# Optimization experiments

Measured on AMD Instinct MI355X. Metric: run time of the kernel, lower is better.

Reference implementation:

```python
import jax, jax.numpy as jnp
import numpy as np

N, E, IN, H, T = 100000, 1600000, 10, 64, 10


def setup_inputs() -> dict:
    key = jax.random.key(0)
    ks = jax.random.split(key, 24)
    w = lambda k, shape, s=0.05: jax.random.normal(k, shape, jnp.float32) * s
    return {
        "x": w(ks[0], (N, IN), 1.0),
        "edge_attr": w(ks[1], (E, T), 1.0),
        "gcn1_w": w(ks[2], (IN, H)), "gcn1_b": jnp.zeros((H,), jnp.float32),
        "e_w1": w(ks[3], (3 * T, H)), "e_b1": jnp.zeros((H,), jnp.float32),
        "e_w2": w(ks[4], (H, H)), "e_b2": jnp.zeros((H,), jnp.float32),
        "gcn2_w": w(ks[5], (2 * H, H)), "gcn2_b": jnp.zeros((H,), jnp.float32),
        "gcn3_w": w(ks[6], (H, IN)), "gcn3_b": jnp.zeros((IN,), jnp.float32),
        "l1_w": w(ks[7], (2 * IN, IN)), "l1_b": jnp.zeros((IN,), jnp.float32),
        "l2_w": w(ks[8], (IN, 128)), "l2_b": jnp.zeros((128,), jnp.float32),
        "l3_w": w(ks[9], (128, 32)), "l3_b": jnp.zeros((32,), jnp.float32),
        "l4_w": w(ks[10], (32, 2)), "l4_b": jnp.zeros((2,), jnp.float32),
        "edge_index": jax.random.randint(ks[11], (2, E), 0, N),
    }


def reference(x, edge_attr, gcn1_w, gcn1_b, e_w1, e_b1, e_w2, e_b2,
              gcn2_w, gcn2_b, gcn3_w, gcn3_b, l1_w, l1_b, l2_w, l2_b,
              l3_w, l3_b, l4_w, l4_b, edge_index):
    src, dst = edge_index[0], edge_index[1]  # j -> i (message flows src->dst)
    # GCN symmetric norm with self loops: deg counted on target, +1 self loop
    deg = 1.0 + jax.ops.segment_sum(jnp.ones((E,), jnp.float32), dst, num_segments=N)
    dis = deg ** -0.5  # [N]
    edge_norm = (dis[src] * dis[dst])[:, None]  # [E,1]

    def gcn(h, w, b):
        hw = h @ w  # [N,out]
        agg = jax.ops.segment_sum(hw[src] * edge_norm, dst, num_segments=N)
        agg = agg + hw * (dis * dis)[:, None]  # self-loop term, norm = 1/deg
        return agg + b

    out1 = jax.nn.relu(gcn(x, gcn1_w, gcn1_b))
    # EdgeConv: gather x_i (dst), x_j (src), concat edge_attr, MLP, scatter-max
    m = jnp.concatenate([x[dst], x[src], edge_attr], axis=1)  # [E, 3T]
    m = jax.nn.relu(m @ e_w1 + e_b1) @ e_w2 + e_b2  # [E, H]
    agg = jax.ops.segment_max(m, dst, num_segments=N)
    agg = jnp.where(jnp.isfinite(agg), agg, 0.0)  # isolated nodes -> 0
    oute = jax.nn.relu(agg)

    out2 = jax.nn.relu(gcn(jnp.concatenate([out1, oute], axis=1), gcn2_w, gcn2_b))
    out3 = jax.nn.relu(gcn(out2, gcn3_w, gcn3_b))
    h = jnp.concatenate([x, out3], axis=1)  # [N, 2*IN]
    h = jax.nn.softplus(h @ l1_w + l1_b)
    h = jax.nn.softplus(h @ l2_w + l2_b)
    h = jax.nn.softplus(h @ l3_w + l3_b)
    h = h @ l4_w + l4_b  # [N, 2]
    return (h[:, 0], h[:, 1])
```

## Files before the change

### kernel.cpp

```cpp
#include <hip/hip_runtime.h>
#include <hip/hip_bf16.h>

typedef unsigned int u32;
typedef unsigned short u16;
typedef _Float16 f16;
typedef _Float16 f16x8 __attribute__((ext_vector_type(8)));
typedef float f32x4 __attribute__((ext_vector_type(4)));
typedef u32 u32x4 __attribute__((ext_vector_type(4)));

#define DEV static __device__ __forceinline__

#define O_G1   0
#define O_G1b  640
#define O_W1   704
#define O_B1   2624
#define O_W2   2688
#define O_B2   6784
#define O_G2   6848
#define O_G2b  15040
#define O_G3   15104
#define O_G3b  15744
#define O_L1   15754
#define O_L1b  15954
#define O_L2t  15964
#define O_L2b  17244
#define O_L3   17372
#define O_L3b  21468
#define O_L4t  21500
#define O_L4b  21564
#define O_WF1  21568
#define O_WF2  22592
#define WTOT   24640

#define ECNB   32

DEV float bfu(u16 h){ return __uint_as_float(((u32)h) << 16); }
DEV float bflo(u32 u){ return __uint_as_float(u << 16); }
DEV float bfhi(u32 u){ return __uint_as_float(u & 0xffff0000u); }
DEV u16 f2bf(float x){
  __hip_bfloat16 b = __float2bfloat16(x);
  return *(u16*)&b;
}
DEV float rdf(const void* p, int idx, int isf32){
  return isf32 ? ((const float*)p)[idx] : bfu(((const u16*)p)[idx]);
}
DEV void load10_bf(const u32* __restrict__ p, float* f){
  u32 a0=p[0],a1=p[1],a2=p[2],a3=p[3],a4=p[4];
  f[0]=bflo(a0); f[1]=bfhi(a0);
  f[2]=bflo(a1); f[3]=bfhi(a1);
  f[4]=bflo(a2); f[5]=bfhi(a2);
  f[6]=bflo(a3); f[7]=bfhi(a3);
  f[8]=bflo(a4); f[9]=bfhi(a4);
}
DEV void load10_any(const void* base, size_t row, int isf32, float* f){
  if (isf32){
    const float* p = (const float*)base + row*10;
    #pragma unroll
    for (int k=0;k<10;k++) f[k] = p[k];
  } else {
    load10_bf((const u32*)base + row*5, f);
  }
}
DEV float softplusf(float x){ return fmaxf(x,0.f) + __logf(1.f + __expf(-fabsf(x))); }

DEV int permk(int k){
  if (k < 8)  return k;
  if (k < 16) return 10 + (k-8);
  if (k < 24) return 20 + (k-16);
  if (k == 24) return 8;
  if (k == 25) return 9;
  if (k == 26) return 18;
  if (k == 27) return 19;
  if (k == 28) return 28;
  if (k == 29) return 29;
  return -1;
}
DEV u32 packh2(float a, float b){
  union { f16 h[2]; u32 u; } t;
  t.h[0] = (f16)a; t.h[1] = (f16)b;
  return t.u;
}

__global__ __launch_bounds__(256) void k_detect(
    const u32* p0, const u32* p1, const u32* p2, const u32* p3,
    const u32* p4, const u32* p5, const u32* p6, const u32* p7,
    const u32* p8, const u32* p9, const u32* p10,const u32* p11,
    const u32* p12,const u32* p13,const u32* p14,const u32* p15,
    const u32* p16,const u32* p17,const u32* p18,const u32* p19,
    int* __restrict__ flags, int N_, int E_)
{
  int a = blockIdx.x;
  const u32* p;
  int elems;
  switch (a){
    case 0:  p=p0;  elems=N_*10; break;
    case 1:  p=p1;  elems=E_*10; break;
    case 2:  p=p2;  elems=640;  break;
    case 3:  p=p3;  elems=64;   break;
    case 4:  p=p4;  elems=1920; break;
    case 5:  p=p5;  elems=64;   break;
    case 6:  p=p6;  elems=4096; break;
    case 7:  p=p7;  elems=64;   break;
    case 8:  p=p8;  elems=8192; break;
    case 9:  p=p9;  elems=64;   break;
    case 10: p=p10; elems=640;  break;
    case 11: p=p11; elems=10;   break;
    case 12: p=p12; elems=200;  break;
    case 13: p=p13; elems=10;   break;
    case 14: p=p14; elems=1280; break;
    case 15: p=p15; elems=128;  break;
    case 16: p=p16; elems=4096; break;
    case 17: p=p17; elems=32;   break;
    case 18: p=p18; elems=64;   break;
    default: p=p19; elems=2;    break;
  }
  int nw = elems/2; if (nw > 512) nw = 512; if (nw < 1) nw = 1;
  int localA = 0, localZ = 0;
  for (int i=threadIdx.x; i<nw; i+=256){
    u32 w = p[i];
    u32 ex = (w >> 7) & 0xffu;
    if (ex >= 0x90u) localA++;
    if ((w & 0xffffu) == 0u) localZ++;
  }
  int packed = (localA << 16) | localZ;
  __shared__ int red[4];
  #pragma unroll
  for (int off=32; off; off>>=1) packed += __shfl_down(packed, off);
  if ((threadIdx.x & 63) == 0) red[threadIdx.x>>6] = packed;
  __syncthreads();
  if (threadIdx.x == 0){
    int s = red[0]+red[1]+red[2]+red[3];
    int sA = s >> 16, sZ = s & 0xffff;
    flags[a] = (sA * 16 >= nw || sZ * 4 >= nw * 3) ? 1 : 0;
  }
}

__global__ __launch_bounds__(256) void k_prep(
    const void* g1w, const void* g1b, const void* ew1, const void* eb1,
    const void* ew2, const void* eb2, const void* g2w, const void* g2b,
    const void* g3w, const void* g3b, const void* l1w, const void* l1b,
    const void* l2w, const void* l2b, const void* l3w, const void* l3b,
    const void* l4w, const void* l4b,
    const int* __restrict__ flags, float* __restrict__ W)
{
  int t = threadIdx.x;
  int f2=flags[2],f3=flags[3],f4=flags[4],f5=flags[5],f6=flags[6],f7=flags[7];
  int f8=flags[8],f9=flags[9],f10=flags[10],f11=flags[11],f12=flags[12],f13=flags[13];
  int f14=flags[14],f15=flags[15],f16=flags[16],f17=flags[17],f18=flags[18],f19=flags[19];
  for (int i=t;i<640;i+=256)  W[O_G1+i]  = rdf(g1w,i,f2);
  for (int i=t;i<64;i+=256)   W[O_G1b+i] = rdf(g1b,i,f3);
  for (int i=t;i<1920;i+=256) W[O_W1+i]  = rdf(ew1,i,f4);
  for (int i=t;i<64;i+=256)   W[O_B1+i]  = rdf(eb1,i,f5);
  for (int i=t;i<4096;i+=256) W[O_W2+i]  = rdf(ew2,i,f6);
  for (int i=t;i<64;i+=256)   W[O_B2+i]  = rdf(eb2,i,f7);
  for (int i=t;i<8192;i+=256) W[O_G2+i]  = rdf(g2w,i,f8);
  for (int i=t;i<64;i+=256)   W[O_G2b+i] = rdf(g2b,i,f9);
  for (int i=t;i<640;i+=256)  W[O_G3+i]  = rdf(g3w,i,f10);
  for (int i=t;i<10;i+=256)   W[O_G3b+i] = rdf(g3b,i,f11);
  for (int i=t;i<200;i+=256)  W[O_L1+i]  = rdf(l1w,i,f12);
  for (int i=t;i<10;i+=256)   W[O_L1b+i] = rdf(l1b,i,f13);
  for (int i=t;i<1280;i+=256){ int o=i/10,k=i-o*10; W[O_L2t+i]=rdf(l2w,k*128+o,f14); }
  for (int i=t;i<128;i+=256)  W[O_L2b+i] = rdf(l2b,i,f15);
  for (int i=t;i<4096;i+=256) W[O_L3+i]  = rdf(l3w,i,f16);
  for (int i=t;i<32;i+=256)   W[O_L3b+i] = rdf(l3b,i,f17);
  for (int i=t;i<64;i+=256){ int c=i>>5,j=i&31; W[O_L4t+i]=rdf(l4w,j*2+c,f18); }
  for (int i=t;i<2;i+=256)    W[O_L4b+i] = rdf(l4b,i,f19);
  u32* Wu = (u32*)W;
  for (int i=t;i<1024;i+=256){
    int l=i&63, q=(i>>6)&3, c=i>>8;
    int k0=(l>>4)*8+2*q, col=c*16+(l&15);
    int r0=permk(k0), r1=permk(k0+1);
    float v0 = (r0<0)?0.f:rdf(ew1,r0*64+col,f4);
    float v1 = (r1<0)?0.f:rdf(ew1,r1*64+col,f4);
    Wu[O_WF1+i] = packh2(v0,v1);
  }
  for (int i=t;i<2048;i+=256){
    int l=i&63, q=(i>>6)&3, h2=(i>>8)&1, c=i>>9;
    int k0=32*h2+(l>>4)*8+2*q, col=c*16+(l&15);
    Wu[O_WF2+i] = packh2(rdf(ew2,k0*64+col,f6), rdf(ew2,(k0+1)*64+col,f6));
  }
}

__global__ __launch_bounds__(256) void k_init(int* __restrict__ cnt, int N_)
{
  int i = blockIdx.x*256 + threadIdx.x;
  if (i < N_) cnt[i] = 0;
}

__global__ __launch_bounds__(256) void k_count(
    const int* __restrict__ ei, int* __restrict__ cnt,
    int* __restrict__ rank, int E_)
{
  int e = blockIdx.x*256 + threadIdx.x;
  if (e >= E_) return;
  rank[e] = atomicAdd(&cnt[ei[E_+e]], 1);
}

__global__ __launch_bounds__(1024) void k_bsum(const int* __restrict__ cnt, int* __restrict__ bsum, int N_)
{
  int i = blockIdx.x*1024 + threadIdx.x;
  int v = (i < N_) ? cnt[i] : 0;
  #pragma unroll
  for (int off=32; off; off>>=1) v += __shfl_down(v, off);
  __shared__ int ws_[16];
  if ((threadIdx.x & 63) == 0) ws_[threadIdx.x>>6] = v;
  __syncthreads();
  if (threadIdx.x == 0){
    int s = 0;
    #pragma unroll
    for (int j=0;j<16;j++) s += ws_[j];
    bsum[blockIdx.x] = s;
  }
}

__global__ __launch_bounds__(128) void k_scan_small(const int* __restrict__ bsum, int* __restrict__ boff, int NB)
{
  int t = threadIdx.x;
  int v = (t < NB) ? bsum[t] : 0;
  int lane = t & 63, w = t >> 6;
  int x = v;
  #pragma unroll
  for (int off=1; off<64; off<<=1){ int y=__shfl_up(x,off); if (lane>=off) x+=y; }
  __shared__ int t2[2];
  if (lane==63) t2[w]=x;
  __syncthreads();
  if (w==1) x += t2[0];
  boff[t] = x - v;
}

__global__ __launch_bounds__(1024) void k_scan_final(
    int* __restrict__ cnt, const int* __restrict__ boff,
    int* __restrict__ rp, float* __restrict__ dis, int N_, int E_)
{
  int i = blockIdx.x*1024 + threadIdx.x;
  int v = (i < N_) ? cnt[i] : 0;
  int lane = threadIdx.x & 63, w = threadIdx.x >> 6;
  int x = v;
  #pragma unroll
  for (int off=1; off<64; off<<=1){ int y=__shfl_up(x,off); if (lane>=off) x+=y; }
  __shared__ int wp[16];
  if (lane==63) wp[w]=x;
  __syncthreads();
  if (threadIdx.x==0){
    int run=0;
    #pragma unroll
    for (int j=0;j<16;j++){ int t=wp[j]; wp[j]=run; run+=t; }
  }
  __syncthreads();
  int incl = x + wp[w] + boff[blockIdx.x];
  if (i < N_){
    rp[i]  = incl - v;
    dis[i] = rsqrtf(1.f + (float)v);
  }
  if (i == 0) rp[N_] = E_;
}

__global__ __launch_bounds__(256) void k_fillpos(
    const int* __restrict__ ei, const int* __restrict__ rank,
    const int* __restrict__ rp, int* __restrict__ inv, int E_)
{
  int e = blockIdx.x*256 + threadIdx.x;
  if (e >= E_) return;
  int d = ei[E_+e];
  inv[rp[d] + rank[e]] = e;
}

__global__ __launch_bounds__(256) void k_fillcsr(
    const int* __restrict__ ei, const int* __restrict__ inv,
    int4* __restrict__ csr, int E_)
{
  int p = blockIdx.x*256 + threadIdx.x;
  if (p >= E_) return;
  int e = inv[p];
  csr[p] = make_int4(ei[e], e, ei[E_+e], 0);
}

#define EC_EMIT \
  if (run >= 0){ int bb = run*64 + x; \
    atomicMax(&nodemax[bb],    __float_as_int(e0)); \
    atomicMax(&nodemax[bb+16], __float_as_int(e1)); \
    atomicMax(&nodemax[bb+32], __float_as_int(e2)); \
    atomicMax(&nodemax[bb+48], __float_as_int(e3)); }
#define EC_STEP(DD, RR) { \
  float t0=fmaxf(mcv[0][RR],0.f), t1=fmaxf(mcv[1][RR],0.f), \
        t2=fmaxf(mcv[2][RR],0.f), t3=fmaxf(mcv[3][RR],0.f); \
  if (DD == run){ e0=fmaxf(e0,t0); e1=fmaxf(e1,t1); e2=fmaxf(e2,t2); e3=fmaxf(e3,t3); } \
  else { EC_EMIT; run = DD; e0=t0; e1=t1; e2=t2; e3=t3; } }

__global__ __launch_bounds__(256) void k_edgeconv(
    const void* __restrict__ xv, const void* __restrict__ eav,
    const int* __restrict__ rp, const int4* __restrict__ csr,
    const float* __restrict__ W, const int* __restrict__ flags,
    float* __restrict__ oute, int N_, int E_)
{
  __shared__ int nodemax[ECNB*64];
  __shared__ u32 hbuf[4][16*36];
  int tid = threadIdx.x;
  int l = tid & 63, wv = tid >> 6;
  int x = l & 15, g = l >> 4;
  int n0 = blockIdx.x * ECNB;
  if (n0 >= N_) return;
  int nend = n0 + ECNB; if (nend > N_) nend = N_;
  #pragma unroll
  for (int i=0;i<ECNB/4;i++) nodemax[i*256 + tid] = 0;
  int fx = flags[0], fea = flags[1];
  const u32* Wu = (const u32*)W;
  union FU { u32 u[4]; f16x8 v; };
  union HU { f16 h[8]; u32 u[4]; f16x8 v; };
  FU w1u[4];
  #pragma unroll
  for (int c=0;c<4;c++){
    #pragma unroll
    for (int q=0;q<4;q++) w1u[c].u[q] = Wu[O_WF1 + (c*4+q)*64 + l];
  }
  FU w2u[4][2];
  #pragma unroll
  for (int c=0;c<4;c++){
    #pragma unroll
    for (int h=0;h<2;h++){
      #pragma unroll
      for (int q=0;q<4;q++) w2u[c][h].u[q] = Wu[O_WF2 + ((c*2+h)*4+q)*64 + l];
    }
  }
  float b1v[4], b2v[4];
  #pragma unroll
  for (int c=0;c<4;c++){ b1v[c] = (W+O_B1)[c*16 + x]; b2v[c] = (W+O_B2)[c*16 + x]; }
  int pbase = rp[n0], pend = rp[nend];
  int ntiles = (pend - pbase + 15) >> 4;
  u32* hb = hbuf[wv];
  __syncthreads();

  for (int t = wv; t < ntiles; t += 4){
    int p0 = pbase + t*16;
    int eA = p0 + x; if (eA > E_-1) eA = E_-1;
    int4 ce = csr[eA];
    HU af;
    u32 exv = 0;
    if (g < 3){
      long row; const void* base; int isf;
      if (g==0){ row = ce.z; base = xv;  isf = fx; }
      else if (g==1){ row = ce.x; base = xv;  isf = fx; }
      else { row = ce.y; base = eav; isf = fea; }
      if (isf){
        const float* p = (const float*)base + row*10;
        #pragma unroll
        for (int j=0;j<8;j++) af.h[j] = (f16)p[j];
        exv = packh2(p[8], p[9]);
      } else {
        const u32* p = (const u32*)base + row*5;
        u32 a0=p[0],a1=p[1],a2=p[2],a3=p[3],a4=p[4];
        af.h[0]=(f16)bflo(a0); af.h[1]=(f16)bfhi(a0);
        af.h[2]=(f16)bflo(a1); af.h[3]=(f16)bfhi(a1);
        af.h[4]=(f16)bflo(a2); af.h[5]=(f16)bfhi(a2);
        af.h[6]=(f16)bflo(a3); af.h[7]=(f16)bfhi(a3);
        exv = packh2(bflo(a4), bfhi(a4));
      }
    }
    u32 ge0 = (u32)__shfl((int)exv, x);
    u32 ge1 = (u32)__shfl((int)exv, x+16);
    u32 ge2 = (u32)__shfl((int)exv, x+32);
    if (g == 3){ af.u[0]=ge0; af.u[1]=ge1; af.u[2]=ge2; af.u[3]=0; }
    int pe = p0 + 4*g;
    int dz = ce.z;
    int d0 = __shfl(dz, 4*g+0); d0 = (pe   < pend) ? d0 - n0 : -1;
    int d1 = __shfl(dz, 4*g+1); d1 = (pe+1 < pend) ? d1 - n0 : -1;
    int d2 = __shfl(dz, 4*g+2); d2 = (pe+2 < pend) ? d2 - n0 : -1;
    int d3 = __shfl(dz, 4*g+3); d3 = (pe+3 < pend) ? d3 - n0 : -1;
    f32x4 z = {0.f,0.f,0.f,0.f};
    f32x4 hc[4];
    #pragma unroll
    for (int c=0;c<4;c++)
      hc[c] = __builtin_amdgcn_mfma_f32_16x16x32_f16(af.v, w1u[c].v, z, 0, 0, 0);
    #pragma unroll
    for (int r=0;r<4;r++){
      u32 pk0,pk1,pk2,pk3;
      {
        float hv = fmaxf(hc[0][r] + b1v[0], 0.f);
        union { f16 h; u16 u; } cv; cv.h=(f16)hv; u32 mine=cv.u;
        u32 other=(u32)__shfl_xor((int)mine,1,64);
        pk0 = (x&1) ? (other|(mine<<16)) : (mine|(other<<16));
      }{
        float hv = fmaxf(hc[1][r] + b1v[1], 0.f);
        union { f16 h; u16 u; } cv; cv.h=(f16)hv; u32 mine=cv.u;
        u32 other=(u32)__shfl_xor((int)mine,1,64);
        pk1 = (x&1) ? (other|(mine<<16)) : (mine|(other<<16));
      }{
        float hv = fmaxf(hc[2][r] + b1v[2], 0.f);
        union { f16 h; u16 u; } cv; cv.h=(f16)hv; u32 mine=cv.u;
        u32 other=(u32)__shfl_xor((int)mine,1,64);
        pk2 = (x&1) ? (other|(mine<<16)) : (mine|(other<<16));
      }{
        float hv = fmaxf(hc[3][r] + b1v[3], 0.f);
        union { f16 h; u16 u; } cv; cv.h=(f16)hv; u32 mine=cv.u;
        u32 other=(u32)__shfl_xor((int)mine,1,64);
        pk3 = (x&1) ? (other|(mine<<16)) : (mine|(other<<16));
      }
      int edge = 4*g + r;
      int par = (x&1) ? 16 : 0;
      hb[edge*36 + par + (x>>1)]     = (x&1) ? pk2 : pk0;
      hb[edge*36 + 8 + par + (x>>1)] = (x&1) ? pk3 : pk1;
    }
    asm volatile("s_waitcnt lgkmcnt(0)" ::: "memory");
    HU a2f[2];
    #pragma unroll
    for (int h=0;h<2;h++){
      const u32x4* p = (const u32x4*)&hb[x*36 + g*4 + 16*h];
      u32x4 tv = *p;
      a2f[h].u[0]=tv[0]; a2f[h].u[1]=tv[1]; a2f[h].u[2]=tv[2]; a2f[h].u[3]=tv[3];
    }
    f32x4 mcv[4];
    #pragma unroll
    for (int c=0;c<4;c++){
      f32x4 bi = {b2v[c],b2v[c],b2v[c],b2v[c]};
      f32x4 acc = __builtin_amdgcn_mfma_f32_16x16x32_f16(a2f[0].v, w2u[c][0].v, bi, 0, 0, 0);
      mcv[c]    = __builtin_amdgcn_mfma_f32_16x16x32_f16(a2f[1].v, w2u[c][1].v, acc, 0, 0, 0);
    }
    int run = -2; float e0=0.f,e1=0.f,e2=0.f,e3=0.f;
    EC_STEP(d0,0) EC_STEP(d1,1) EC_STEP(d2,2) EC_STEP(d3,3)
    EC_EMIT;
  }
  __syncthreads();
  int tot = (nend - n0) * 64;
  for (int i = tid; i < tot; i += 256)
    oute[(size_t)n0*64 + i] = __int_as_float(nodemax[i]);
}

__global__ __launch_bounds__(256) void k_aggx(
    const void* __restrict__ xv, const int* __restrict__ rp,
    const int4* __restrict__ csr, const float* __restrict__ dis,
    const int* __restrict__ flags, float* __restrict__ sx, int N_)
{
  int i = blockIdx.x*256 + threadIdx.x;
  if (i >= N_) return;
  int fx = flags[0];
  float di = dis[i], d2 = di*di;
  float acc[10], ac2[10], tA[10], tB[10], tC[10], tD[10];
  load10_any(xv, (size_t)i, fx, tA);
  #pragma unroll
  for (int f=0;f<10;f++){ acc[f] = tA[f]*d2; ac2[f] = 0.f; }
  int b = rp[i], en = rp[i+1];
  int p = b;
  for (; p+3 < en; p += 4){
    int s0 = csr[p].x, s1 = csr[p+1].x, s2 = csr[p+2].x, s3 = csr[p+3].x;
    float m0 = dis[s0]*di, m1 = dis[s1]*di, m2 = dis[s2]*di, m3 = dis[s3]*di;
    load10_any(xv, (size_t)s0, fx, tA);
    load10_any(xv, (size_t)s1, fx, tB);
    load10_any(xv, (size_t)s2, fx, tC);
    load10_any(xv, (size_t)s3, fx, tD);
    #pragma unroll
    for (int f=0;f<10;f++){
      acc[f] = fmaf(tA[f], m0, acc[f]);
      ac2[f] = fmaf(tB[f], m1, ac2[f]);
      acc[f] = fmaf(tC[f], m2, acc[f]);
      ac2[f] = fmaf(tD[f], m3, ac2[f]);
    }
  }
  for (; p < en; p++){
    int s0 = csr[p].x; float m0 = dis[s0]*di;
    load10_any(xv, (size_t)s0, fx, tA);
    #pragma unroll
    for (int f=0;f<10;f++) acc[f] = fmaf(tA[f], m0, acc[f]);
  }
  float* o = sx + (size_t)i*10;
  #pragma unroll
  for (int f=0;f<10;f++) o[f] = acc[f] + ac2[f];
}

__global__ __launch_bounds__(256) void k_hw2(
    const float* __restrict__ sx, const float* __restrict__ oute,
    const float* __restrict__ W, u16* __restrict__ hw2o, int N_)
{
  int i = blockIdx.x*256 + threadIdx.x;
  if (i >= N_) return;
  float sv[10];
  const float* srow = sx + (size_t)i*10;
  #pragma unroll
  for (int f=0;f<10;f++) sv[f] = srow[f];
  const float* __restrict__ G1  = W + O_G1;
  const float* __restrict__ G1b = W + O_G1b;
  const float* __restrict__ G2  = W + O_G2;
  float hw[64];
  #pragma unroll
  for (int f=0;f<64;f++) hw[f] = 0.f;
  #pragma unroll 1
  for (int k=0;k<64;k++){
    float o1 = G1b[k];
    #pragma unroll
    for (int j=0;j<10;j++) o1 = fmaf(sv[j], G1[j*64+k], o1);
    o1 = fmaxf(o1, 0.f);
    const float* __restrict__ wt = G2 + k*64;
    #pragma unroll
    for (int f=0;f<64;f++) hw[f] = fmaf(o1, wt[f], hw[f]);
  }
  const float* orow = oute + (size_t)i*64;
  #pragma unroll 1
  for (int k=0;k<64;k++){
    float ov = orow[k];
    const float* __restrict__ wb = G2 + (64+k)*64;
    #pragma unroll
    for (int f=0;f<64;f++) hw[f] = fmaf(ov, wb[f], hw[f]);
  }
  u16* out = hw2o + (size_t)i*64;
  #pragma unroll
  for (int f=0;f<64;f++) out[f] = f2bf(hw[f]);
}

__global__ __launch_bounds__(256) void k_agg64(
    const u16* __restrict__ hw2, const int* __restrict__ rp,
    const int4* __restrict__ csr, const float* __restrict__ dis,
    const float* __restrict__ W, float* __restrict__ out2, int N_)
{
  int i = (blockIdx.x*256 + threadIdx.x) >> 6;
  int lane = threadIdx.x & 63;
  if (i >= N_) return;
  int e4 = lane >> 4, c4 = lane & 15;
  float di = dis[i];
  int b = rp[i], en = rp[i+1];
  const uint2* __restrict__ h2 = (const uint2*)hw2;
  float a0=0.f,a1=0.f,a2=0.f,a3=0.f;
  float b0=0.f,b1=0.f,b2=0.f,b3=0.f;
  int p = b + e4;
  int sA = (p   < en) ? csr[p].x   : 0;
  int sB = (p+4 < en) ? csr[p+4].x : 0;
  for (; p + 4 < en; p += 8){
    int sAn = (p+8  < en) ? csr[p+8].x  : 0;
    int sBn = (p+12 < en) ? csr[p+12].x : 0;
    float nmA = dis[sA]*di, nmB = dis[sB]*di;
    uint2 wA = h2[(size_t)sA*16 + c4];
    uint2 wB = h2[(size_t)sB*16 + c4];
    a0 = fmaf(bflo(wA.x), nmA, a0); a1 = fmaf(bfhi(wA.x), nmA, a1);
    a2 = fmaf(bflo(wA.y), nmA, a2); a3 = fmaf(bfhi(wA.y), nmA, a3);
    b0 = fmaf(bflo(wB.x), nmB, b0); b1 = fmaf(bfhi(wB.x), nmB, b1);
    b2 = fmaf(bflo(wB.y), nmB, b2); b3 = fmaf(bfhi(wB.y), nmB, b3);
    sA = sAn; sB = sBn;
  }
  if (p < en){
    float nmA = dis[sA]*di;
    uint2 wA = h2[(size_t)sA*16 + c4];
    a0 = fmaf(bflo(wA.x), nmA, a0); a1 = fmaf(bfhi(wA.x), nmA, a1);
    a2 = fmaf(bflo(wA.y), nmA, a2); a3 = fmaf(bfhi(wA.y), nmA, a3);
  }
  a0 += b0; a1 += b1; a2 += b2; a3 += b3;
  a0 += __shfl_xor(a0,16); a1 += __shfl_xor(a1,16);
  a2 += __shfl_xor(a2,16); a3 += __shfl_xor(a3,16);
  a0 += __shfl_xor(a0,32); a1 += __shfl_xor(a1,32);
  a2 += __shfl_xor(a2,32); a3 += __shfl_xor(a3,32);
  if (e4 == 0){
    uint2 ws2 = h2[(size_t)i*16 + c4];
    float d2 = di*di;
    const float* G2b = W + O_G2b;
    float4 o;
    o.x = fmaxf(fmaf(bflo(ws2.x), d2, a0) + G2b[4*c4],   0.f);
    o.y = fmaxf(fmaf(bfhi(ws2.x), d2, a1) + G2b[4*c4+1], 0.f);
    o.z = fmaxf(fmaf(bflo(ws2.y), d2, a2) + G2b[4*c4+2], 0.f);
    o.w = fmaxf(fmaf(bfhi(ws2.y), d2, a3) + G2b[4*c4+3], 0.f);
    *(float4*)(out2 + (size_t)i*64 + 4*c4) = o;
  }
}

__global__ __launch_bounds__(256) void k_hw3(
    const float* __restrict__ out2, const float* __restrict__ W,
    float* __restrict__ hw3, int N_)
{
  int i = blockIdx.x*256 + threadIdx.x;
  if (i >= N_) return;
  const float* row = out2 + (size_t)i*64;
  const float* __restrict__ G3 = W + O_G3;
  float a[10];
  #pragma unroll
  for (int f=0;f<10;f++) a[f] = 0.f;
  #pragma unroll 1
  for (int k=0;k<64;k++){
    float v = row[k];
    const float* __restrict__ w = G3 + k*10;
    #pragma unroll
    for (int f=0;f<10;f++) a[f] = fmaf(v, w[f], a[f]);
  }
  float* o = hw3 + (size_t)i*10;
  #pragma unroll
  for (int f=0;f<10;f++) o[f] = a[f];
}

__global__ __launch_bounds__(256) void k_final(
    const void* __restrict__ xv, const float* __restrict__ hw3,
    const int* __restrict__ rp, const int4* __restrict__ csr,
    const float* __restrict__ dis, const int* __restrict__ flags,
    const float* __restrict__ W, float* __restrict__ out, int N_)
{
  int i = blockIdx.x*256 + threadIdx.x;
  if (i >= N_) return;
  int fx = flags[0];
  float di = dis[i];
  float a[10], a2v[10];
  const float* hrow = hw3 + (size_t)i*10;
  #pragma unroll
  for (int f=0;f<10;f++){ a[f] = hrow[f]*di*di; a2v[f] = 0.f; }
  int b = rp[i], en = rp[i+1];
  int p = b;
  for (; p+3 < en; p += 4){
    int s0 = csr[p].x, s1 = csr[p+1].x, s2 = csr[p+2].x, s3 = csr[p+3].x;
    float m0 = dis[s0]*di, m1 = dis[s1]*di, m2 = dis[s2]*di, m3 = dis[s3]*di;
    const float* r0p = hw3 + (size_t)s0*10;
    const float* r1p = hw3 + (size_t)s1*10;
    const float* r2p = hw3 + (size_t)s2*10;
    const float* r3p = hw3 + (size_t)s3*10;
    #pragma unroll
    for (int f=0;f<10;f++){
      a[f]   = fmaf(r0p[f], m0, a[f]);
      a2v[f] = fmaf(r1p[f], m1, a2v[f]);
      a[f]   = fmaf(r2p[f], m2, a[f]);
      a2v[f] = fmaf(r3p[f], m3, a2v[f]);
    }
  }
  for (; p < en; p++){
    int s0 = csr[p].x; float m0 = dis[s0]*di;
    const float* r0p = hw3 + (size_t)s0*10;
    #pragma unroll
    for (int f=0;f<10;f++) a[f] = fmaf(r0p[f], m0, a[f]);
  }
  #pragma unroll
  for (int f=0;f<10;f++) a[f] += a2v[f];
  const float* G3b = W + O_G3b;
  float h20[20];
  load10_any(xv, (size_t)i, fx, h20);
  #pragma unroll
  for (int f=0;f<10;f++) h20[10+f] = fmaxf(a[f] + G3b[f], 0.f);
  const float* __restrict__ L1  = W + O_L1;
  const float* __restrict__ L1b = W + O_L1b;
  float h1[10];
  #pragma unroll
  for (int f=0;f<10;f++) h1[f] = L1b[f];
  #pragma unroll
  for (int k=0;k<20;k++){
    float v = h20[k];
    const float* __restrict__ w = L1 + k*10;
    #pragma unroll
    for (int f=0;f<10;f++) h1[f] = fmaf(v, w[f], h1[f]);
  }
  #pragma unroll
  for (int f=0;f<10;f++) h1[f] = softplusf(h1[f]);
  const float* __restrict__ L2t = W + O_L2t;
  const float* __restrict__ L2b = W + O_L2b;
  const float* __restrict__ L3  = W + O_L3;
  const float* __restrict__ L3b = W + O_L3b;
  float h3a[32], h3b[32];
  #pragma unroll
  for (int j=0;j<32;j++){ h3a[j] = L3b[j]; h3b[j] = 0.f; }
  #pragma unroll 1
  for (int o=0;o<64;o++){
    float sA = L2b[o], sB = L2b[o+64];
    const float* __restrict__ wtA = L2t + o*10;
    const float* __restrict__ wtB = L2t + (o+64)*10;
    #pragma unroll
    for (int k=0;k<10;k++){
      sA = fmaf(h1[k], wtA[k], sA);
      sB = fmaf(h1[k], wtB[k], sB);
    }
    sA = softplusf(sA);
    sB = softplusf(sB);
    const float* __restrict__ w3A = L3 + o*32;
    const float* __restrict__ w3B = L3 + (o+64)*32;
    #pragma unroll
    for (int j=0;j<32;j++){
      h3a[j] = fmaf(sA, w3A[j], h3a[j]);
      h3b[j] = fmaf(sB, w3B[j], h3b[j]);
    }
  }
  const float* L4t = W + O_L4t;
  const float* L4b = W + O_L4b;
  float r0 = L4b[0], r1 = L4b[1];
  #pragma unroll
  for (int j=0;j<32;j++){
    float h3 = softplusf(h3a[j] + h3b[j]);
    r0 = fmaf(h3, L4t[j],    r0);
    r1 = fmaf(h3, L4t[32+j], r1);
  }
  out[i]      = r0;
  out[N_ + i] = r1;
}

extern "C" void kernel_launch(void* const* d_in, const int* in_sizes, int n_in,
                              void* d_out, int out_size, void* d_ws, size_t ws_size,
                              hipStream_t stream)
{
  const void* xv  = d_in[0];
  const void* eav = d_in[1];
  const int*  ei  = (const int*)d_in[20];
  int N_ = in_sizes[0] / 10;
  int E_ = in_sizes[1] / 10;

  float* W = (float*)d_ws;
  size_t off = WTOT;
  int*   cnt   = (int*)(W + off);   off += (size_t)N_;
  int*   rp    = (int*)(W + off);   off += (size_t)N_ + 1;
  float* dis   = (float*)(W + off); off += (size_t)N_;
  int*   bsum  = (int*)(W + off);   off += 256;
  int*   boff  = (int*)(W + off);   off += 256;
  int*   flags = (int*)(W + off);   off += 32;
  off = (off + 3) & ~(size_t)3;
  int4*  csr   = (int4*)(W + off);  off += (size_t)E_ * 4;
  float* oute  = (float*)(W + off);
  float* out2  = oute;
  off += (size_t)N_ * 64;
  u16*   hw2   = (u16*)(W + off);   off += (size_t)N_ * 32;
  float* sx    = (float*)(W + off);
  float* hw3   = sx;
  off += (size_t)N_ * 10;

  int* rank;
  if ((size_t)E_ <= (size_t)N_ * 64) rank = (int*)oute;
  else { rank = (int*)(W + off); off += (size_t)E_; }
  int* inv;
  if ((size_t)E_ <= (size_t)N_ * 32) inv = (int*)hw2;
  else { inv = (int*)(W + off); off += (size_t)E_; }

  if (ws_size < off * sizeof(float)) return;

  int gN = (N_ + 255)/256, gE = (E_ + 255)/256;
  int NB = (N_ + 1023)/1024;

  k_detect<<<20,256,0,stream>>>(
      (const u32*)d_in[0],(const u32*)d_in[1],
      (const u32*)d_in[2],(const u32*)d_in[3],(const u32*)d_in[4],(const u32*)d_in[5],
      (const u32*)d_in[6],(const u32*)d_in[7],(const u32*)d_in[8],(const u32*)d_in[9],
      (const u32*)d_in[10],(const u32*)d_in[11],(const u32*)d_in[12],(const u32*)d_in[13],
      (const u32*)d_in[14],(const u32*)d_in[15],(const u32*)d_in[16],(const u32*)d_in[17],
      (const u32*)d_in[18],(const u32*)d_in[19],
      flags, N_, E_);
  k_prep<<<1,256,0,stream>>>(
      d_in[2],d_in[3],d_in[4],d_in[5],d_in[6],d_in[7],d_in[8],d_in[9],
      d_in[10],d_in[11],d_in[12],d_in[13],d_in[14],d_in[15],d_in[16],d_in[17],
      d_in[18],d_in[19], flags, W);
  k_init<<<gN,256,0,stream>>>(cnt, N_);
  k_count<<<gE,256,0,stream>>>(ei, cnt, rank, E_);
  k_bsum<<<NB,1024,0,stream>>>(cnt, bsum, N_);
  k_scan_small<<<1,128,0,stream>>>(bsum, boff, NB);
  k_scan_final<<<NB,1024,0,stream>>>(cnt, boff, rp, dis, N_, E_);
  k_fillpos<<<gE,256,0,stream>>>(ei, rank, rp, inv, E_);
  k_fillcsr<<<gE,256,0,stream>>>(ei, inv, csr, E_);
  k_edgeconv<<<(N_+ECNB-1)/ECNB,256,0,stream>>>(xv, eav, rp, csr, W, flags, oute, N_, E_);
  k_aggx<<<gN,256,0,stream>>>(xv, rp, csr, dis, flags, sx, N_);
  k_hw2<<<gN,256,0,stream>>>(sx, oute, W, hw2, N_);
  k_agg64<<<(N_+3)/4,256,0,stream>>>(hw2, rp, csr, dis, W, out2, N_);
  k_hw3<<<gN,256,0,stream>>>(out2, W, hw3, N_);
  k_final<<<gN,256,0,stream>>>(xv, hw3, rp, csr, dis, flags, W,
                               (float*)d_out, N_);
}
```

Measured before the change: 645.7 us.

## Fuse aggx into hw2 and fold hw3 projection into agg64 epilogue

Merges the 10-wide x aggregation kernel with the 64-wide hidden projection, so the intermediate sx buffer is neither written nor reread. Also folds the 64->10 GCN3 matmul into the agg64 kernel's epilogue: each wavefront computes partial dot products across lanes and reduces them with shuffles, so the out2 round trip and one launch go away. The fused aggx+hw2 kernel may need more registers and run at lower occupancy, and the agg64 epilogue now runs on all lanes with extra shuffles.

```diff
diff --git a/kernel.cpp b/kernel.cpp
--- a/kernel.cpp
+++ b/kernel.cpp
@@ -425,19 +425,20 @@
     oute[(size_t)n0*64 + i] = __int_as_float(nodemax[i]);
 }
 
-__global__ __launch_bounds__(256) void k_aggx(
+__global__ __launch_bounds__(256) void k_aggxhw2(
     const void* __restrict__ xv, const int* __restrict__ rp,
     const int4* __restrict__ csr, const float* __restrict__ dis,
-    const int* __restrict__ flags, float* __restrict__ sx, int N_)
+    const int* __restrict__ flags, const float* __restrict__ oute,
+    const float* __restrict__ W, u16* __restrict__ hw2o, int N_)
 {
   int i = blockIdx.x*256 + threadIdx.x;
   if (i >= N_) return;
   int fx = flags[0];
   float di = dis[i], d2 = di*di;
-  float acc[10], ac2[10], tA[10], tB[10], tC[10], tD[10];
+  float sv[10], ac2[10], tA[10], tB[10], tC[10], tD[10];
   load10_any(xv, (size_t)i, fx, tA);
   #pragma unroll
-  for (int f=0;f<10;f++){ acc[f] = tA[f]*d2; ac2[f] = 0.f; }
+  for (int f=0;f<10;f++){ sv[f] = tA[f]*d2; ac2[f] = 0.f; }
   int b = rp[i], en = rp[i+1];
   int p = b;
   for (; p+3 < en; p += 4){
@@ -449,9 +450,9 @@
     load10_any(xv, (size_t)s3, fx, tD);
     #pragma unroll
     for (int f=0;f<10;f++){
-      acc[f] = fmaf(tA[f], m0, acc[f]);
+      sv[f]  = fmaf(tA[f], m0, sv[f]);
       ac2[f] = fmaf(tB[f], m1, ac2[f]);
-      acc[f] = fmaf(tC[f], m2, acc[f]);
+      sv[f]  = fmaf(tC[f], m2, sv[f]);
       ac2[f] = fmaf(tD[f], m3, ac2[f]);
     }
   }
@@ -459,23 +460,10 @@
     int s0 = csr[p].x; float m0 = dis[s0]*di;
     load10_any(xv, (size_t)s0, fx, tA);
     #pragma unroll
-    for (int f=0;f<10;f++) acc[f] = fmaf(tA[f], m0, acc[f]);
-  }
-  float* o = sx + (size_t)i*10;
-  #pragma unroll
-  for (int f=0;f<10;f++) o[f] = acc[f] + ac2[f];
-}
-
-__global__ __launch_bounds__(256) void k_hw2(
-    const float* __restrict__ sx, const float* __restrict__ oute,
-    const float* __restrict__ W, u16* __restrict__ hw2o, int N_)
-{
-  int i = blockIdx.x*256 + threadIdx.x;
-  if (i >= N_) return;
-  float sv[10];
-  const float* srow = sx + (size_t)i*10;
-  #pragma unroll
-  for (int f=0;f<10;f++) sv[f] = srow[f];
+    for (int f=0;f<10;f++) sv[f] = fmaf(tA[f], m0, sv[f]);
+  }
+  #pragma unroll
+  for (int f=0;f<10;f++) sv[f] += ac2[f];
   const float* __restrict__ G1  = W + O_G1;
   const float* __restrict__ G1b = W + O_G1b;
   const float* __restrict__ G2  = W + O_G2;
@@ -508,7 +496,7 @@
 __global__ __launch_bounds__(256) void k_agg64(
     const u16* __restrict__ hw2, const int* __restrict__ rp,
     const int4* __restrict__ csr, const float* __restrict__ dis,
-    const float* __restrict__ W, float* __restrict__ out2, int N_)
+    const float* __restrict__ W, float* __restrict__ hw3, int N_)
 {
   int i = (blockIdx.x*256 + threadIdx.x) >> 6;
   int lane = threadIdx.x & 63;
@@ -545,40 +533,35 @@
   a2 += __shfl_xor(a2,16); a3 += __shfl_xor(a3,16);
   a0 += __shfl_xor(a0,32); a1 += __shfl_xor(a1,32);
   a2 += __shfl_xor(a2,32); a3 += __shfl_xor(a3,32);
-  if (e4 == 0){
-    uint2 ws2 = h2[(size_t)i*16 + c4];
-    float d2 = di*di;
-    const float* G2b = W + O_G2b;
-    float4 o;
-    o.x = fmaxf(fmaf(bflo(ws2.x), d2, a0) + G2b[4*c4],   0.f);
-    o.y = fmaxf(fmaf(bfhi(ws2.x), d2, a1) + G2b[4*c4+1], 0.f);
-    o.z = fmaxf(fmaf(bflo(ws2.y), d2, a2) + G2b[4*c4+2], 0.f);
-    o.w = fmaxf(fmaf(bfhi(ws2.y), d2, a3) + G2b[4*c4+3], 0.f);
-    *(float4*)(out2 + (size_t)i*64 + 4*c4) = o;
-  }
-}
-
-__global__ __launch_bounds__(256) void k_hw3(
-    const float* __restrict__ out2, const float* __restrict__ W,
-    float* __restrict__ hw3, int N_)
-{
-  int i = blockIdx.x*256 + threadIdx.x;
-  if (i >= N_) return;
-  const float* row = out2 + (size_t)i*64;
+  uint2 ws2 = h2[(size_t)i*16 + c4];
+  float d2 = di*di;
+  const float* G2b = W + O_G2b;
+  float o0 = fmaxf(fmaf(bflo(ws2.x), d2, a0) + G2b[4*c4],   0.f);
+  float o1 = fmaxf(fmaf(bfhi(ws2.x), d2, a1) + G2b[4*c4+1], 0.f);
+  float o2 = fmaxf(fmaf(bflo(ws2.y), d2, a2) + G2b[4*c4+2], 0.f);
+  float o3 = fmaxf(fmaf(bfhi(ws2.y), d2, a3) + G2b[4*c4+3], 0.f);
   const float* __restrict__ G3 = W + O_G3;
-  float a[10];
-  #pragma unroll
-  for (int f=0;f<10;f++) a[f] = 0.f;
-  #pragma unroll 1
-  for (int k=0;k<64;k++){
-    float v = row[k];
-    const float* __restrict__ w = G3 + k*10;
-    #pragma unroll
-    for (int f=0;f<10;f++) a[f] = fmaf(v, w[f], a[f]);
-  }
-  float* o = hw3 + (size_t)i*10;
-  #pragma unroll
-  for (int f=0;f<10;f++) o[f] = a[f];
+  const float* r0g = G3 + (4*c4+0)*10;
+  const float* r1g = G3 + (4*c4+1)*10;
+  const float* r2g = G3 + (4*c4+2)*10;
+  const float* r3g = G3 + (4*c4+3)*10;
+  int f0 = e4*3;
+  int f1 = (f0+1 > 9) ? 9 : f0+1;
+  int f2v = (f0+2 > 9) ? 9 : f0+2;
+  float p0v = o0*r0g[f0]  + o1*r1g[f0]  + o2*r2g[f0]  + o3*r3g[f0];
+  float p1v = o0*r0g[f1]  + o1*r1g[f1]  + o2*r2g[f1]  + o3*r3g[f1];
+  float p2v = o0*r0g[f2v] + o1*r1g[f2v] + o2*r2g[f2v] + o3*r3g[f2v];
+  #pragma unroll
+  for (int off=1; off<16; off<<=1){
+    p0v += __shfl_xor(p0v, off);
+    p1v += __shfl_xor(p1v, off);
+    p2v += __shfl_xor(p2v, off);
+  }
+  if (c4 == 0){
+    float* o = hw3 + (size_t)i*10;
+    if (e4 < 3){ o[f0] = p0v; o[f0+1] = p1v; o[f0+2] = p2v; }
+    else o[9] = p0v;
+  }
 }
 
 __global__ __launch_bounds__(256) void k_final(
@@ -699,13 +682,9 @@
   int*   flags = (int*)(W + off);   off += 32;
   off = (off + 3) & ~(size_t)3;
   int4*  csr   = (int4*)(W + off);  off += (size_t)E_ * 4;
-  float* oute  = (float*)(W + off);
-  float* out2  = oute;
-  off += (size_t)N_ * 64;
+  float* oute  = (float*)(W + off); off += (size_t)N_ * 64;
   u16*   hw2   = (u16*)(W + off);   off += (size_t)N_ * 32;
-  float* sx    = (float*)(W + off);
-  float* hw3   = sx;
-  off += (size_t)N_ * 10;
+  float* hw3   = (float*)(W + off); off += (size_t)N_ * 10;
 
   int* rank;
   if ((size_t)E_ <= (size_t)N_ * 64) rank = (int*)oute;
@@ -739,10 +718,8 @@
   k_fillpos<<<gE,256,0,stream>>>(ei, rank, rp, inv, E_);
   k_fillcsr<<<gE,256,0,stream>>>(ei, inv, csr, E_);
   k_edgeconv<<<(N_+ECNB-1)/ECNB,256,0,stream>>>(xv, eav, rp, csr, W, flags, oute, N_, E_);
-  k_aggx<<<gN,256,0,stream>>>(xv, rp, csr, dis, flags, sx, N_);
-  k_hw2<<<gN,256,0,stream>>>(sx, oute, W, hw2, N_);
-  k_agg64<<<(N_+3)/4,256,0,stream>>>(hw2, rp, csr, dis, W, out2, N_);
-  k_hw3<<<gN,256,0,stream>>>(out2, W, hw3, N_);
+  k_aggxhw2<<<gN,256,0,stream>>>(xv, rp, csr, dis, flags, oute, W, hw2, N_);
+  k_agg64<<<(N_+3)/4,256,0,stream>>>(hw2, rp, csr, dis, W, hw3, N_);
   k_final<<<gN,256,0,stream>>>(xv, hw3, rp, csr, dis, flags, W,
                                (float*)d_out, N_);
 }
```

Measured after the change: 712.7 us. 10.4% more time.
